# Performance work log

Hardware: AMD Instinct MI355X
Metric: run time of the kernel (lower is better)

## Reference

```python
import jax, jax.numpy as jnp
from jax import lax
import numpy as np

# Dims
B_, CIN, COUT, T = 2, 64, 128, 8192
K, NM, N, DCONV, EXP = 5, 2, 16, 4, 2   # kernel, n_mamba, d_state, d_conv, expand
DI = EXP * COUT                          # d_inner = 256
DTR = (COUT + 15) // 16                  # dt_rank = 8
M = NM * 2                               # mamba instances (fwd+bwd per block)


def setup_inputs() -> dict:
    key = jax.random.key(0)
    ks = jax.random.split(key, 8)
    r = lambda k, s, sc=0.02: (jax.random.normal(k, s) * sc).astype(jnp.float32)
    return {
        "x": jax.random.normal(ks[0], (B_, CIN, T), dtype=jnp.float32),
        "conv_w": r(ks[1], (COUT, CIN, K), 0.05),
        "conv_b": jnp.zeros((COUT,), jnp.float32),
        "gn_g": jnp.ones((COUT,), jnp.float32),
        "gn_b": jnp.zeros((COUT,), jnp.float32),
        "prelu_a": jnp.full((1,), 0.25, jnp.float32),
        "ln_g": jnp.ones((NM, COUT), jnp.float32),
        "ln_b": jnp.zeros((NM, COUT), jnp.float32),
        "W_in": r(ks[2], (M, 2 * DI, COUT)),
        "conv1d_w": r(ks[3], (M, DI, 1, DCONV), 0.1),
        "conv1d_b": jnp.zeros((M, DI), jnp.float32),
        "W_xproj": r(ks[4], (M, DTR + 2 * N, DI)),
        "W_dt": r(ks[5], (M, DI, DTR), 0.1),
        "b_dt": jnp.full((M, DI), -4.0, jnp.float32),
        "A_log": jnp.broadcast_to(jnp.log(jnp.arange(1, N + 1, dtype=jnp.float32)), (M, DI, N)).copy(),
        "D_param": jnp.ones((M, DI), jnp.float32),
        "W_out": r(ks[6], (M, COUT, DI)),
    }


def _silu(x):
    return x * jax.nn.sigmoid(x)


def _layernorm(x, g, b, eps=1e-5):
    mu = x.mean(-1, keepdims=True)
    v = ((x - mu) ** 2).mean(-1, keepdims=True)
    return (x - mu) * lax.rsqrt(v + eps) * g + b


def _mamba(h, Wi, cw, cb, Wx, Wd, bd, Alog, Dp, Wo):
    # h: [B, L, d_model] -> [B, L, d_model]. Standard Mamba (S6) block.
    Bb, L, _ = h.shape
    xz = jnp.einsum('bld,ed->ble', h, Wi)               # [B,L,2*DI]
    xp, z = jnp.split(xz, 2, axis=-1)
    xc = jnp.transpose(xp, (0, 2, 1))                   # [B,DI,L]
    xc = lax.conv_general_dilated(xc, cw, (1,), [(DCONV - 1, 0)],
                                  feature_group_count=DI,
                                  dimension_numbers=('NCH', 'OIH', 'NCH')) + cb[None, :, None]
    u = _silu(jnp.transpose(xc, (0, 2, 1)))             # [B,L,DI]
    xdbl = jnp.einsum('bld,ed->ble', u, Wx)             # [B,L,DTR+2N]
    dt, Bm, Cm = jnp.split(xdbl, [DTR, DTR + N], axis=-1)
    delta = jax.nn.softplus(jnp.einsum('blr,dr->bld', dt, Wd) + bd)  # [B,L,DI]
    A = -jnp.exp(Alog)                                  # [DI,N]
    dA = jnp.exp(delta[..., None] * A)                  # [B,L,DI,N]
    dBu = (delta * u)[..., None] * Bm[:, :, None, :]    # [B,L,DI,N]

    def step(hc, inp):
        a, b, c = inp
        hc = a * hc + b                                  # [B,DI,N]
        return hc, jnp.einsum('bdn,bn->bd', hc, c)

    h0 = jnp.zeros((Bb, DI, N), dtype=h.dtype)
    _, ys = lax.scan(step, h0, (jnp.moveaxis(dA, 1, 0), jnp.moveaxis(dBu, 1, 0), jnp.moveaxis(Cm, 1, 0)))
    y = jnp.moveaxis(ys, 0, 1) + u * Dp                 # [B,L,DI]
    y = y * _silu(z)
    return jnp.einsum('ble,de->bld', y, Wo)


def reference(x, conv_w, conv_b, gn_g, gn_b, prelu_a, ln_g, ln_b, W_in,
              conv1d_w, conv1d_b, W_xproj, W_dt, b_dt, A_log, D_param, W_out):
    # Conv1d stride 2, padding K//2: [B,CIN,T] -> [B,COUT,T//2]
    h = lax.conv_general_dilated(x, conv_w, (2,), [(K // 2, K // 2)],
                                 dimension_numbers=('NCH', 'OIH', 'NCH')) + conv_b[None, :, None]
    # GroupNorm(1, COUT): normalize jointly over (C, T)
    mu = h.mean((1, 2), keepdims=True)
    v = ((h - mu) ** 2).mean((1, 2), keepdims=True)
    h = (h - mu) * lax.rsqrt(v + 1e-5) * gn_g[None, :, None] + gn_b[None, :, None]
    h = jnp.where(h >= 0, h, prelu_a[0] * h)            # PReLU (shared scalar)
    h = jnp.transpose(h, (0, 2, 1))                     # [B, L, C]
    for i in range(NM):
        hn = _layernorm(h, ln_g[i], ln_b[i])
        f, bw = 2 * i, 2 * i + 1
        yf = _mamba(hn, W_in[f], conv1d_w[f], conv1d_b[f], W_xproj[f], W_dt[f], b_dt[f], A_log[f], D_param[f], W_out[f])
        hb = jnp.flip(hn, axis=1)
        yb = jnp.flip(_mamba(hb, W_in[bw], conv1d_w[bw], conv1d_b[bw], W_xproj[bw], W_dt[bw], b_dt[bw], A_log[bw], D_param[bw], W_out[bw]), axis=1)
        h = h + yf + yb                                  # bidirectional residual
    return jnp.transpose(h, (0, 2, 1))                   # [B, COUT, T//2]
```

## Files before the change

### kernel.cpp

```cpp
#include <hip/hip_runtime.h>
#include <hip/hip_bf16.h>
#include <math.h>

constexpr int B2   = 2;
constexpr int CIN  = 64;
constexpr int COUT = 128;
constexpr int T    = 8192;
constexpr int L    = 4096;
constexpr int DI   = 256;
constexpr int NST  = 16;
constexpr int DTR  = 8;
constexpr int Q    = 32;
constexpr int NC   = 128;
constexpr int TOK  = B2 * L;

typedef __attribute__((ext_vector_type(8))) short bf16x8s;
typedef __attribute__((ext_vector_type(4))) float f32x4;

__device__ __forceinline__ float sigmoidf_(float x) { return 1.f / (1.f + __expf(-x)); }
__device__ __forceinline__ unsigned short f2bf(float f) {
    unsigned int u = __float_as_uint(f);
    unsigned int r = (u + 0x7FFFu + ((u >> 16) & 1u)) >> 16;
    return (unsigned short)r;
}
__device__ __forceinline__ float bf2f(unsigned short s) {
    return __uint_as_float((unsigned int)s << 16);
}

__global__ __launch_bounds__(256) void prep_all_kernel(
    const float* __restrict__ W_in, const float* __restrict__ W_out,
    const float* __restrict__ cw,
    unsigned short* __restrict__ Winb, unsigned short* __restrict__ Woutb,
    unsigned short* __restrict__ Wrb, float* __restrict__ stats) {
    int idx = blockIdx.x * 256 + threadIdx.x;
    if (blockIdx.x == 0 && threadIdx.x < 4) stats[threadIdx.x] = 0.f;
    if (idx < 262144) {
        Winb[idx] = f2bf(W_in[idx]);
    } else if (idx < 393216) {
        int i = idx - 262144; Woutb[i] = f2bf(W_out[i]);
    } else if (idx < 434176) {
        int i = idx - 393216;
        int co = i / 320, r = i % 320;
        int kp = r >> 6, ci = r & 63;
        Wrb[i] = f2bf(cw[co * 320 + ci * 5 + kp]);
    }
}

__global__ __launch_bounds__(256) void xpose_kernel(
    const float* __restrict__ x, unsigned short* __restrict__ xTb) {
    __shared__ float tile[64][65];
    int b = blockIdx.y, tb = blockIdx.x * 64, tid = threadIdx.x;
    #pragma unroll
    for (int i = 0; i < 16; ++i) {
        int idx = i * 256 + tid; int ci = idx >> 6, tt = idx & 63;
        tile[ci][tt] = x[((size_t)b * CIN + ci) * T + tb + tt];
    }
    __syncthreads();
    #pragma unroll
    for (int i = 0; i < 16; ++i) {
        int idx = i * 256 + tid; int tt = idx >> 6, ci = idx & 63;
        xTb[((size_t)b * T + tb + tt) * 64 + ci] = f2bf(tile[ci][tt]);
    }
}

__global__ __launch_bounds__(256) void conv_mfma_kernel(
    const unsigned short* __restrict__ xTb, const unsigned short* __restrict__ Wrb,
    const float* __restrict__ cb, float* __restrict__ h, float* __restrict__ stats) {
    const int tid = threadIdx.x;
    const int w = tid >> 6, lane = tid & 63, q = lane >> 4, c = lane & 15;
    const int t0g = blockIdx.x * 64;
    const int t0  = t0g + w * 16;
    const int ct0 = blockIdx.y * 64;
    const int b   = t0g >> 12;
    const int l   = (t0 + c) & (L - 1);
    f32x4 acc[4] = {};
    for (int kc = 0; kc < 320; kc += 32) {
        int kp  = kc >> 6;
        int ci0 = (kc & 63) + q * 8;
        int p = 2 * l + kp - 2;
        bf16x8s a = {};
        if (p >= 0 && p < T)
            a = *(const bf16x8s*)&xTb[((size_t)b * T + p) * 64 + ci0];
        #pragma unroll
        for (int i = 0; i < 4; ++i) {
            bf16x8s bb = *(const bf16x8s*)&Wrb[(size_t)(ct0 + i * 16 + c) * 320 + kc + q * 8];
            acc[i] = __builtin_amdgcn_mfma_f32_16x16x32_bf16(a, bb, acc[i], 0, 0, 0);
        }
    }
    float s = 0.f, ss = 0.f;
    #pragma unroll
    for (int i = 0; i < 4; ++i) {
        int cout = ct0 + i * 16 + c;
        float bias = cb[cout];
        #pragma unroll
        for (int r = 0; r < 4; ++r) {
            int tok = t0 + q * 4 + r;
            float v = acc[i][r] + bias;
            h[(size_t)tok * COUT + cout] = v;
            s += v; ss += v * v;
        }
    }
    #pragma unroll
    for (int off = 32; off; off >>= 1) {
        s  += __shfl_down(s,  off, 64);
        ss += __shfl_down(ss, off, 64);
    }
    if (lane == 0) {
        atomicAdd(&stats[b * 2 + 0], s);
        atomicAdd(&stats[b * 2 + 1], ss);
    }
}

__global__ __launch_bounds__(256) void gn_ln_kernel(
    float* __restrict__ h, const float* __restrict__ gn_g,
    const float* __restrict__ gn_b, const float* __restrict__ prelu_a,
    const float* __restrict__ stats, unsigned short* __restrict__ hnb,
    const float* __restrict__ lng, const float* __restrict__ lnb) {
    int wave = threadIdx.x >> 6, lane = threadIdx.x & 63;
    int t = blockIdx.x * 4 + wave;
    int b = t >> 12;
    const float n = (float)(L * COUT);
    float mu   = stats[b * 2 + 0] / n;
    float var  = stats[b * 2 + 1] / n - mu * mu;
    float rstd = rsqrtf(var + 1e-5f);
    float a = prelu_a[0];
    float* row = h + (size_t)t * COUT;
    float2 v  = *(const float2*)&row[lane * 2];
    float2 g  = *(const float2*)&gn_g[lane * 2];
    float2 bb = *(const float2*)&gn_b[lane * 2];
    v.x = (v.x - mu) * rstd * g.x + bb.x; v.x = v.x >= 0.f ? v.x : a * v.x;
    v.y = (v.y - mu) * rstd * g.y + bb.y; v.y = v.y >= 0.f ? v.y : a * v.y;
    *(float2*)&row[lane * 2] = v;
    float s = v.x + v.y, ss = v.x * v.x + v.y * v.y;
    #pragma unroll
    for (int off = 32; off; off >>= 1) {
        s  += __shfl_xor(s,  off, 64);
        ss += __shfl_xor(ss, off, 64);
    }
    float mu2 = s * (1.f / 128.f);
    float var2 = ss * (1.f / 128.f) - mu2 * mu2;
    float rstd2 = rsqrtf(var2 + 1e-5f);
    float2 gg = *(const float2*)&lng[lane * 2];
    float2 lb = *(const float2*)&lnb[lane * 2];
    ushort2 o;
    o.x = f2bf((v.x - mu2) * rstd2 * gg.x + lb.x);
    o.y = f2bf((v.y - mu2) * rstd2 * gg.y + lb.y);
    *(ushort2*)&hnb[(size_t)t * COUT + lane * 2] = o;
}

__global__ __launch_bounds__(256) void ln_kernel(
    const float* __restrict__ h, unsigned short* __restrict__ hnb,
    const float* __restrict__ g, const float* __restrict__ bta) {
    int wave = threadIdx.x >> 6, lane = threadIdx.x & 63;
    int t = blockIdx.x * 4 + wave;
    const float* row = h + (size_t)t * COUT;
    float2 v = *(const float2*)&row[lane * 2];
    float s = v.x + v.y, ss = v.x * v.x + v.y * v.y;
    #pragma unroll
    for (int off = 32; off; off >>= 1) {
        s  += __shfl_xor(s,  off, 64);
        ss += __shfl_xor(ss, off, 64);
    }
    float mu = s * (1.f / 128.f);
    float var = ss * (1.f / 128.f) - mu * mu;
    float rstd = rsqrtf(var + 1e-5f);
    float2 gg = *(const float2*)&g[lane * 2];
    float2 bb = *(const float2*)&bta[lane * 2];
    ushort2 o;
    o.x = f2bf((v.x - mu) * rstd * gg.x + bb.x);
    o.y = f2bf((v.y - mu) * rstd * gg.y + bb.y);
    *(ushort2*)&hnb[(size_t)t * COUT + lane * 2] = o;
}

__global__ __launch_bounds__(256) void inproj_dw_kernel(
    const unsigned short* __restrict__ hnb, const unsigned short* __restrict__ Winb,
    const float* __restrict__ cw, const float* __restrict__ cbias,
    float* __restrict__ u0, float* __restrict__ u1,
    unsigned short* __restrict__ zb0, unsigned short* __restrict__ zb1, int layer) {
    __shared__ float xs[80 * 68];
    const int tid = threadIdx.x;
    const int w = tid >> 6, lane = tid & 63, q = lane >> 4, c = lane & 15;
    const int tBase = blockIdx.x * 64;
    const int nBase = blockIdx.y * 64;
    const int inst = nBase >> 9;
    const int e0 = nBase & 511;
    const int m = layer * 2 + inst;
    const unsigned short* Wb = Winb + (size_t)m * 512 * 128;

    if (e0 >= 256) {
        const int t0 = tBase + w * 16;
        f32x4 acc[4] = {};
        for (int kc = 0; kc < 128; kc += 32) {
            bf16x8s a = *(const bf16x8s*)&hnb[(size_t)(t0 + c) * 128 + kc + q * 8];
            #pragma unroll
            for (int i = 0; i < 4; ++i) {
                bf16x8s bb = *(const bf16x8s*)&Wb[(size_t)(e0 + i * 16 + c) * 128 + kc + q * 8];
                acc[i] = __builtin_amdgcn_mfma_f32_16x16x32_bf16(a, bb, acc[i], 0, 0, 0);
            }
        }
        unsigned short* zb = inst ? zb1 : zb0;
        #pragma unroll
        for (int i = 0; i < 4; ++i) {
            int eo = (e0 + i * 16 + c) & 255;
            #pragma unroll
            for (int r = 0; r < 4; ++r) {
                int tok = t0 + q * 4 + r;
                float v = acc[i][r];
                zb[(size_t)tok * DI + eo] = f2bf(v * sigmoidf_(v));
            }
        }
        return;
    }
    const int winT0 = (inst == 0) ? (tBase - 16) : tBase;
    for (int pass = 0; pass < 2; ++pass) {
        if (pass == 1 && w != 0) break;
        int slot = (pass == 0) ? (w + (inst == 0 ? 1 : 0))
                               : ((inst == 0) ? 0 : 4);
        int tokA = winT0 + slot * 16 + c;
        tokA = tokA < 0 ? 0 : (tokA > TOK - 1 ? TOK - 1 : tokA);
        f32x4 acc[4] = {};
        for (int kc = 0; kc < 128; kc += 32) {
            bf16x8s a = *(const bf16x8s*)&hnb[(size_t)tokA * 128 + kc + q * 8];
            #pragma unroll
            for (int i = 0; i < 4; ++i) {
                bf16x8s bb = *(const bf16x8s*)&Wb[(size_t)(e0 + i * 16 + c) * 128 + kc + q * 8];
                acc[i] = __builtin_amdgcn_mfma_f32_16x16x32_bf16(a, bb, acc[i], 0, 0, 0);
            }
        }
        #pragma unroll
        for (int i = 0; i < 4; ++i)
            #pragma unroll
            for (int r = 0; r < 4; ++r)
                xs[(slot * 16 + q * 4 + r) * 68 + i * 16 + c] = acc[i][r];
    }
    __syncthreads();
    const int l0base = tBase & (L - 1);
    const int ch4 = tid & 15;
    const int d0 = e0 + ch4 * 4;
    float4 w0 = *(const float4*)&cw[(size_t)(m * DI + d0 + 0) * 4];
    float4 w1 = *(const float4*)&cw[(size_t)(m * DI + d0 + 1) * 4];
    float4 w2 = *(const float4*)&cw[(size_t)(m * DI + d0 + 2) * 4];
    float4 w3 = *(const float4*)&cw[(size_t)(m * DI + d0 + 3) * 4];
    float4 bias4 = *(const float4*)&cbias[m * DI + d0];
    float* ud = inst ? u1 : u0;
    #pragma unroll
    for (int p = 0; p < 4; ++p) {
        int j = p * 16 + (tid >> 4);
        float4 acc = bias4;
        #pragma unroll
        for (int k = 0; k < 4; ++k) {
            bool valid = (inst == 0) ? (l0base + j - 3 + k >= 0)
                                     : (l0base + j + 3 - k < L);
            if (valid) {
                int wj = (inst == 0) ? (j + 13 + k) : (j + 3 - k);
                float4 v = *(const float4*)&xs[wj * 68 + ch4 * 4];
                float wk0 = ((const float*)&w0)[k], wk1 = ((const float*)&w1)[k];
                float wk2 = ((const float*)&w2)[k], wk3 = ((const float*)&w3)[k];
                acc.x = fmaf(wk0, v.x, acc.x); acc.y = fmaf(wk1, v.y, acc.y);
                acc.z = fmaf(wk2, v.z, acc.z); acc.w = fmaf(wk3, v.w, acc.w);
            }
        }
        acc.x *= sigmoidf_(acc.x); acc.y *= sigmoidf_(acc.y);
        acc.z *= sigmoidf_(acc.z); acc.w *= sigmoidf_(acc.w);
        *(float4*)&ud[(size_t)(tBase + j) * DI + d0] = acc;
    }
}

__global__ __launch_bounds__(256) void xproj_kernel(
    const float* __restrict__ u0, const float* __restrict__ u1,
    const float* __restrict__ Wx, const float* __restrict__ Wdt,
    const float* __restrict__ bdt,
    float* __restrict__ dl0, float* __restrict__ dl1,
    float* __restrict__ Bm0, float* __restrict__ Bm1,
    float* __restrict__ Cm0, float* __restrict__ Cm1, int layer) {
    __shared__ float Ws[40 * 132];
    __shared__ float As[128 * 33];
    __shared__ float xd[32 * 9];
    const int tid   = threadIdx.x;
    const int tBase = blockIdx.x * 32;
    const int inst  = blockIdx.y;
    const int m     = layer * 2 + inst;
    const float* u  = inst ? u1 : u0;
    const float* Wm = Wx + (size_t)m * 40 * 256;
    const int t  = tid & 31;
    const int eq = tid >> 5;
    float acc[5] = {};
    for (int kc = 0; kc < 256; kc += 128) {
        __syncthreads();
        #pragma unroll
        for (int i = 0; i < 5; ++i) {
            int idx = i * 256 + tid;
            int e = idx >> 5, kq = idx & 31;
            float4 w4 = *(const float4*)&Wm[(size_t)e * 256 + kc + kq * 4];
            float* dstw = &Ws[e * 132 + kq * 4];
            dstw[0] = w4.x; dstw[1] = w4.y; dstw[2] = w4.z; dstw[3] = w4.w;
        }
        #pragma unroll
        for (int i = 0; i < 4; ++i) {
            int flat = i * 256 + tid;
            int tt = flat >> 5, kq = flat & 31;
            float4 v = *(const float4*)&u[(size_t)(tBase + tt) * DI + kc + kq * 4];
            As[(kq * 4 + 0) * 33 + tt] = v.x;
            As[(kq * 4 + 1) * 33 + tt] = v.y;
            As[(kq * 4 + 2) * 33 + tt] = v.z;
            As[(kq * 4 + 3) * 33 + tt] = v.w;
        }
        __syncthreads();
        #pragma unroll 4
        for (int kk = 0; kk < 128; ++kk) {
            float a = As[kk * 33 + t];
            acc[0] = fmaf(a, Ws[(eq     ) * 132 + kk], acc[0]);
            acc[1] = fmaf(a, Ws[(eq +  8) * 132 + kk], acc[1]);
            acc[2] = fmaf(a, Ws[(eq + 16) * 132 + kk], acc[2]);
            acc[3] = fmaf(a, Ws[(eq + 24) * 132 + kk], acc[3]);
            acc[4] = fmaf(a, Ws[(eq + 32) * 132 + kk], acc[4]);
        }
    }
    {
        int tok = tBase + t;
        float* Bm = inst ? Bm1 : Bm0;
        float* Cm = inst ? Cm1 : Cm0;
        xd[t * 9 + eq] = acc[0];
        Bm[(size_t)tok * NST + eq]     = acc[1];
        Bm[(size_t)tok * NST + 8 + eq] = acc[2];
        Cm[(size_t)tok * NST + eq]     = acc[3];
        Cm[(size_t)tok * NST + 8 + eq] = acc[4];
    }
    __syncthreads();
    {
        int d = tid;
        float wr[8];
        #pragma unroll
        for (int r = 0; r < 8; ++r) wr[r] = Wdt[((size_t)m * DI + d) * DTR + r];
        float bb = bdt[m * DI + d];
        float* dl = inst ? dl1 : dl0;
        #pragma unroll 4
        for (int tt = 0; tt < 32; ++tt) {
            float a2 = bb;
            #pragma unroll
            for (int r = 0; r < 8; ++r) a2 = fmaf(xd[tt * 9 + r], wr[r], a2);
            float sp = fmaxf(a2, 0.f) + __logf(1.f + __expf(-fabsf(a2)));
            dl[(size_t)(tBase + tt) * DI + d] = sp;
        }
    }
}

__global__ __launch_bounds__(256) void scan1_kernel(
    const float* __restrict__ dl0, const float* __restrict__ dl1,
    const float* __restrict__ u0,  const float* __restrict__ u1,
    const float* __restrict__ Bm0, const float* __restrict__ Bm1,
    const float* __restrict__ A_log,
    float* __restrict__ hend, float* __restrict__ dsumb, int layer) {
    const int tid = threadIdx.x;
    const int nq = tid & 3, dlane = tid >> 2;
    const int chunk = blockIdx.x & (NC - 1), dtile = blockIdx.x >> 7;
    const int b = blockIdx.y, inst = blockIdx.z;
    const int m = layer * 2 + inst, dir = inst;
    const int d = dtile * 64 + dlane;
    const float* dl = inst ? dl1 : dl0;
    const float* u  = inst ? u1  : u0;
    const float* Bm = inst ? Bm1 : Bm0;
    float4 av = *(const float4*)&A_log[((size_t)m * DI + d) * NST + nq * 4];
    const float a0 = -expf(av.x), a1 = -expf(av.y), a2 = -expf(av.z), a3 = -expf(av.w);
    const int s0 = chunk * Q;
    const int l0 = dir ? (L - 1 - s0) : s0;
    const int stp = dir ? -1 : 1;
    long iDU = ((long)(b * L + l0)) * DI + d;
    int  iB  = ((b * L + l0) << 4) + nq * 4;
    const long sDU = (long)stp * DI;
    const int  sB  = stp * NST;
    float h0 = 0.f, h1 = 0.f, h2 = 0.f, h3 = 0.f, dsum = 0.f;
    #pragma unroll 4
    for (int t = 0; t < Q; ++t) {
        float dlt = dl[iDU], uu = u[iDU];
        float4 bm = *(const float4*)&Bm[iB];
        float du = dlt * uu;
        h0 = fmaf(__expf(dlt * a0), h0, du * bm.x);
        h1 = fmaf(__expf(dlt * a1), h1, du * bm.y);
        h2 = fmaf(__expf(dlt * a2), h2, du * bm.z);
        h3 = fmaf(__expf(dlt * a3), h3, du * bm.w);
        dsum += dlt;
        iDU += sDU; iB += sB;
    }
    size_t oh = (((size_t)(inst * 2 + b) * DI + d) * NC + chunk) * NST + nq * 4;
    *(float4*)&hend[oh] = make_float4(h0, h1, h2, h3);
    if (nq == 0) dsumb[((size_t)(inst * 2 + b) * NC + chunk) * DI + d] = dsum;
}

__global__ __launch_bounds__(256) void combine_kernel(
    float* __restrict__ hend, const float* __restrict__ dsumb,
    const float* __restrict__ A_log, int layer) {
    int flat = blockIdx.x * 256 + threadIdx.x;
    int n = flat & 15;
    int d = (flat >> 4) & 255;
    int b = (flat >> 12) & 1;
    int inst = flat >> 13;
    int m = layer * 2 + inst;
    float a = -expf(A_log[((size_t)m * DI + d) * NST + n]);
    size_t baseE = (((size_t)(inst * 2 + b) * DI + d) * NC) * NST + n;
    size_t baseD = ((size_t)(inst * 2 + b) * NC) * DI + d;
    float hc = 0.f;
    #pragma unroll 4
    for (int c = 0; c < NC; ++c) {
        float tmp = hend[baseE + (size_t)c * NST];
        hend[baseE + (size_t)c * NST] = hc;
        float ds = dsumb[baseD + (size_t)c * DI];
        hc = fmaf(__expf(a * ds), hc, tmp);
    }
}

__global__ __launch_bounds__(256) void scan2_kernel(
    const float* __restrict__ dl0, const float* __restrict__ dl1,
    const float* __restrict__ u0,  const float* __restrict__ u1,
    const float* __restrict__ Bm0, const float* __restrict__ Bm1,
    const float* __restrict__ Cm0, const float* __restrict__ Cm1,
    unsigned short* __restrict__ zb0, unsigned short* __restrict__ zb1,
    const float* __restrict__ hin, const float* __restrict__ A_log,
    const float* __restrict__ Dp, int layer) {
    const int tid = threadIdx.x;
    const int nq = tid & 3, dlane = tid >> 2;
    const int chunk = blockIdx.x & (NC - 1), dtile = blockIdx.x >> 7;
    const int b = blockIdx.y, inst = blockIdx.z;
    const int m = layer * 2 + inst, dir = inst;
    const int d = dtile * 64 + dlane;
    const float* dl = inst ? dl1 : dl0;
    const float* u  = inst ? u1  : u0;
    const float* Bm = inst ? Bm1 : Bm0;
    const float* Cm = inst ? Cm1 : Cm0;
    unsigned short* zs = inst ? zb1 : zb0;
    float4 av = *(const float4*)&A_log[((size_t)m * DI + d) * NST + nq * 4];
    const float a0 = -expf(av.x), a1 = -expf(av.y), a2 = -expf(av.z), a3 = -expf(av.w);
    const float dpar = Dp[m * DI + d];
    const int s0 = chunk * Q;
    const int l0 = dir ? (L - 1 - s0) : s0;
    const int stp = dir ? -1 : 1;
    long iDU = ((long)(b * L + l0)) * DI + d;
    int  iB  = ((b * L + l0) << 4) + nq * 4;
    const long sDU = (long)stp * DI;
    const int  sB  = stp * NST;
    float4 hv = *(const float4*)&hin[(((size_t)(inst * 2 + b) * DI + d) * NC + chunk) * NST + nq * 4];
    float h0 = hv.x, h1 = hv.y, h2 = hv.z, h3 = hv.w;
    #pragma unroll 4
    for (int t = 0; t < Q; ++t) {
        float dlt = dl[iDU], uu = u[iDU];
        float4 bm = *(const float4*)&Bm[iB];
        float4 cm = *(const float4*)&Cm[iB];
        float du = dlt * uu;
        h0 = fmaf(__expf(dlt * a0), h0, du * bm.x);
        h1 = fmaf(__expf(dlt * a1), h1, du * bm.y);
        h2 = fmaf(__expf(dlt * a2), h2, du * bm.z);
        h3 = fmaf(__expf(dlt * a3), h3, du * bm.w);
        float yp = h0 * cm.x + h1 * cm.y + h2 * cm.z + h3 * cm.w;
        yp += __shfl_xor(yp, 1, 4);
        yp += __shfl_xor(yp, 2, 4);
        if (nq == 0) {
            float zv = bf2f(zs[iDU]);
            zs[iDU] = f2bf(fmaf(uu, dpar, yp) * zv);
        }
        iDU += sDU; iB += sB;
    }
}

__global__ __launch_bounds__(256) void outproj_mfma_kernel(
    const unsigned short* __restrict__ ygb0, const unsigned short* __restrict__ ygb1,
    const unsigned short* __restrict__ Woutb, float* __restrict__ h, int layer) {
    const int tid = threadIdx.x;
    const int w = tid >> 6, lane = tid & 63, q = lane >> 4, c = lane & 15;
    const int t0 = blockIdx.x * 64 + w * 16;
    const int ct0 = blockIdx.y * 32;
    f32x4 acc[2] = {};
    #pragma unroll
    for (int inst = 0; inst < 2; ++inst) {
        const unsigned short* yg = inst ? ygb1 : ygb0;
        const unsigned short* Wb = Woutb + (size_t)(layer * 2 + inst) * COUT * DI;
        for (int kc = 0; kc < 256; kc += 32) {
            bf16x8s a = *(const bf16x8s*)&yg[(size_t)(t0 + c) * DI + kc + q * 8];
            #pragma unroll
            for (int i = 0; i < 2; ++i) {
                bf16x8s bb = *(const bf16x8s*)&Wb[(size_t)(ct0 + i * 16 + c) * DI + kc + q * 8];
                acc[i] = __builtin_amdgcn_mfma_f32_16x16x32_bf16(a, bb, acc[i], 0, 0, 0);
            }
        }
    }
    #pragma unroll
    for (int i = 0; i < 2; ++i) {
        int cout = ct0 + i * 16 + c;
        #pragma unroll
        for (int r = 0; r < 4; ++r) {
            int tok = t0 + q * 4 + r;
            h[(size_t)tok * COUT + cout] += acc[i][r];
        }
    }
}

__global__ __launch_bounds__(256) void transpose_kernel(
    const float* __restrict__ h, float* __restrict__ out) {
    __shared__ float tile[32][33];
    int lt0 = blockIdx.x * 32, ct0 = blockIdx.y * 32, b = blockIdx.z;
    int c = threadIdx.x & 31, r = threadIdx.x >> 5;
    #pragma unroll
    for (int j = 0; j < 4; ++j) {
        int ll = r + 8 * j;
        tile[ll][c] = h[((size_t)b * L + lt0 + ll) * COUT + ct0 + c];
    }
    __syncthreads();
    #pragma unroll
    for (int j = 0; j < 4; ++j) {
        int cc = r + 8 * j;
        out[((size_t)b * COUT + ct0 + cc) * L + lt0 + c] = tile[c][cc];
    }
}

extern "C" void kernel_launch(void* const* d_in, const int* in_sizes, int n_in,
                              void* d_out, int out_size, void* d_ws, size_t ws_size,
                              hipStream_t stream) {
    const float* x        = (const float*)d_in[0];
    const float* conv_w   = (const float*)d_in[1];
    const float* conv_b   = (const float*)d_in[2];
    const float* gn_g     = (const float*)d_in[3];
    const float* gn_b     = (const float*)d_in[4];
    const float* prelu_a  = (const float*)d_in[5];
    const float* ln_g     = (const float*)d_in[6];
    const float* ln_b     = (const float*)d_in[7];
    const float* W_in     = (const float*)d_in[8];
    const float* conv1d_w = (const float*)d_in[9];
    const float* conv1d_b = (const float*)d_in[10];
    const float* W_xproj  = (const float*)d_in[11];
    const float* W_dt     = (const float*)d_in[12];
    const float* b_dt     = (const float*)d_in[13];
    const float* A_log    = (const float*)d_in[14];
    const float* D_param  = (const float*)d_in[15];
    const float* W_out    = (const float*)d_in[16];

    float* ws = (float*)d_ws;
    float* h     = ws;
    unsigned short* zb0 = (unsigned short*)(ws + 5242880);
    unsigned short* zb1 = (unsigned short*)(ws + 6291456);
    float* u0    = ws + 7340032;
    float* u1    = ws + 9437184;
    float* dl0   = ws + 11534336;
    float* dl1   = ws + 13631488;
    float* Bm0   = ws + 15728640;
    float* Bm1   = ws + 15859712;
    float* Cm0   = ws + 15990784;
    float* Cm1   = ws + 16121856;
    float* hend  = ws + 16252928;
    float* dsumb = ws + 18350080;
    unsigned short* Winb  = (unsigned short*)(ws + 18481152);
    unsigned short* Wrb   = (unsigned short*)(ws + 18612224);
    unsigned short* Woutb = (unsigned short*)(ws + 18632704);
    float* stats = ws + 18698240;
    unsigned short* hnb = (unsigned short*)hend;
    unsigned short* xTb = zb0;

    prep_all_kernel<<<1696, 256, 0, stream>>>(W_in, W_out, conv_w, Winb, Woutb, Wrb, stats);
    xpose_kernel<<<dim3(T / 64, B2), 256, 0, stream>>>(x, xTb);
    conv_mfma_kernel<<<dim3(TOK / 64, COUT / 64), 256, 0, stream>>>(xTb, Wrb, conv_b, h, stats);
    gn_ln_kernel<<<TOK / 4, 256, 0, stream>>>(h, gn_g, gn_b, prelu_a, stats, hnb, ln_g, ln_b);

    for (int layer = 0; layer < 2; ++layer) {
        if (layer == 1)
            ln_kernel<<<TOK / 4, 256, 0, stream>>>(h, hnb, ln_g + COUT, ln_b + COUT);
        inproj_dw_kernel<<<dim3(TOK / 64, 16), 256, 0, stream>>>(hnb, Winb, conv1d_w, conv1d_b,
                                                                 u0, u1, zb0, zb1, layer);
        xproj_kernel<<<dim3(TOK / 32, 2), 256, 0, stream>>>(u0, u1, W_xproj, W_dt, b_dt,
                                                            dl0, dl1, Bm0, Bm1, Cm0, Cm1, layer);
        scan1_kernel<<<dim3(NC * 4, B2, 2), 256, 0, stream>>>(dl0, dl1, u0, u1, Bm0, Bm1,
                                                              A_log, hend, dsumb, layer);
        combine_kernel<<<64, 256, 0, stream>>>(hend, dsumb, A_log, layer);
        scan2_kernel<<<dim3(NC * 4, B2, 2), 256, 0, stream>>>(dl0, dl1, u0, u1, Bm0, Bm1, Cm0, Cm1,
                                                              zb0, zb1, hend, A_log, D_param, layer);
        outproj_mfma_kernel<<<dim3(TOK / 64, 4), 256, 0, stream>>>(zb0, zb1, Woutb, h, layer);
    }
    transpose_kernel<<<dim3(L / 32, COUT / 32, B2), 256, 0, stream>>>(h, (float*)d_out);
}
```

Baseline: 379.8 us.

## Recompute delta in scan kernels, restructure xproj, fuse final transpose into outproj

The xproj kernel no longer materialises the full [TOK, DI] softplus delta tensor. It writes only the 8-wide dt-rank projection, and both scan kernels recompute delta per chunk in shared memory from xd, W_dt and b_dt. This removes a large write and two large reads of delta per layer, at the cost of duplicated softplus work in scan1 and scan2. The xproj GEMM is also rewritten to read operands directly from global memory with register tiling and a split-K reduction in shared memory. The last layer's outproj writes the transposed output directly, which drops the separate transpose kernel.

```diff
diff --git a/kernel.cpp b/kernel.cpp
--- a/kernel.cpp
+++ b/kernel.cpp
@@ -268,103 +268,128 @@
 
 __global__ __launch_bounds__(256) void xproj_kernel(
     const float* __restrict__ u0, const float* __restrict__ u1,
-    const float* __restrict__ Wx, const float* __restrict__ Wdt,
-    const float* __restrict__ bdt,
-    float* __restrict__ dl0, float* __restrict__ dl1,
+    const float* __restrict__ Wx,
+    float* __restrict__ xd0, float* __restrict__ xd1,
     float* __restrict__ Bm0, float* __restrict__ Bm1,
     float* __restrict__ Cm0, float* __restrict__ Cm1, int layer) {
-    __shared__ float Ws[40 * 132];
-    __shared__ float As[128 * 33];
-    __shared__ float xd[32 * 9];
+    __shared__ float red[4][64][21];
     const int tid   = threadIdx.x;
+    const int kq    = tid >> 6;
+    const int lane  = tid & 63;
+    const int eq    = lane & 7;
+    const int tq    = lane >> 3;
     const int tBase = blockIdx.x * 32;
     const int inst  = blockIdx.y;
     const int m     = layer * 2 + inst;
     const float* u  = inst ? u1 : u0;
     const float* Wm = Wx + (size_t)m * 40 * 256;
-    const int t  = tid & 31;
-    const int eq = tid >> 5;
-    float acc[5] = {};
-    for (int kc = 0; kc < 256; kc += 128) {
-        __syncthreads();
-        #pragma unroll
-        for (int i = 0; i < 5; ++i) {
-            int idx = i * 256 + tid;
-            int e = idx >> 5, kq = idx & 31;
-            float4 w4 = *(const float4*)&Wm[(size_t)e * 256 + kc + kq * 4];
-            float* dstw = &Ws[e * 132 + kq * 4];
-            dstw[0] = w4.x; dstw[1] = w4.y; dstw[2] = w4.z; dstw[3] = w4.w;
-        }
-        #pragma unroll
-        for (int i = 0; i < 4; ++i) {
-            int flat = i * 256 + tid;
-            int tt = flat >> 5, kq = flat & 31;
-            float4 v = *(const float4*)&u[(size_t)(tBase + tt) * DI + kc + kq * 4];
-            As[(kq * 4 + 0) * 33 + tt] = v.x;
-            As[(kq * 4 + 1) * 33 + tt] = v.y;
-            As[(kq * 4 + 2) * 33 + tt] = v.z;
-            As[(kq * 4 + 3) * 33 + tt] = v.w;
-        }
-        __syncthreads();
-        #pragma unroll 4
-        for (int kk = 0; kk < 128; ++kk) {
-            float a = As[kk * 33 + t];
-            acc[0] = fmaf(a, Ws[(eq     ) * 132 + kk], acc[0]);
-            acc[1] = fmaf(a, Ws[(eq +  8) * 132 + kk], acc[1]);
-            acc[2] = fmaf(a, Ws[(eq + 16) * 132 + kk], acc[2]);
-            acc[3] = fmaf(a, Ws[(eq + 24) * 132 + kk], acc[3]);
-            acc[4] = fmaf(a, Ws[(eq + 32) * 132 + kk], acc[4]);
-        }
-    }
+    const int k0 = kq * 64;
+    const float* uB = u + (size_t)(tBase + tq * 4) * 256 + k0;
+    float acc[5][4] = {};
+    #pragma unroll 2
+    for (int kk = 0; kk < 64; kk += 4) {
+        float4 a[4], w[5];
+        #pragma unroll
+        for (int j = 0; j < 4; ++j)
+            a[j] = *(const float4*)&uB[(size_t)j * 256 + kk];
+        #pragma unroll
+        for (int i = 0; i < 5; ++i)
+            w[i] = *(const float4*)&Wm[(size_t)(eq + i * 8) * 256 + k0 + kk];
+        #pragma unroll
+        for (int i = 0; i < 5; ++i)
+            #pragma unroll
+            for (int j = 0; j < 4; ++j) {
+                acc[i][j] = fmaf(a[j].x, w[i].x, acc[i][j]);
+                acc[i][j] = fmaf(a[j].y, w[i].y, acc[i][j]);
+                acc[i][j] = fmaf(a[j].z, w[i].z, acc[i][j]);
+                acc[i][j] = fmaf(a[j].w, w[i].w, acc[i][j]);
+            }
+    }
+    #pragma unroll
+    for (int i = 0; i < 5; ++i)
+        #pragma unroll
+        for (int j = 0; j < 4; ++j)
+            red[kq][lane][i * 4 + j] = acc[i][j];
+    __syncthreads();
+    if (kq != 0) return;
+    #pragma unroll
+    for (int i = 0; i < 5; ++i)
+        #pragma unroll
+        for (int j = 0; j < 4; ++j)
+            acc[i][j] = red[0][lane][i * 4 + j] + red[1][lane][i * 4 + j]
+                      + red[2][lane][i * 4 + j] + red[3][lane][i * 4 + j];
+    float* xd = inst ? xd1 : xd0;
+    float* Bm = inst ? Bm1 : Bm0;
+    float* Cm = inst ? Cm1 : Cm0;
+    #pragma unroll
+    for (int j = 0; j < 4; ++j) {
+        int tok = tBase + tq * 4 + j;
+        xd[(size_t)tok * DTR + eq]       = acc[0][j];
+        Bm[(size_t)tok * NST + eq]       = acc[1][j];
+        Bm[(size_t)tok * NST + 8 + eq]   = acc[2][j];
+        Cm[(size_t)tok * NST + eq]       = acc[3][j];
+        Cm[(size_t)tok * NST + 8 + eq]   = acc[4][j];
+    }
+}
+
+__device__ __forceinline__ void compute_dls(
+    const float* __restrict__ xd, const float* __restrict__ Wdt,
+    const float* __restrict__ bdt, int m, int dtile, int b, int l0, int stp,
+    float* dls, float* xdL, float* WdtL, float* bdtL) {
+    const int tid = threadIdx.x;
     {
-        int tok = tBase + t;
-        float* Bm = inst ? Bm1 : Bm0;
-        float* Cm = inst ? Cm1 : Cm0;
-        xd[t * 9 + eq] = acc[0];
-        Bm[(size_t)tok * NST + eq]     = acc[1];
-        Bm[(size_t)tok * NST + 8 + eq] = acc[2];
-        Cm[(size_t)tok * NST + eq]     = acc[3];
-        Cm[(size_t)tok * NST + 8 + eq] = acc[4];
+        int j = tid >> 3, r = tid & 7;
+        xdL[j * 9 + r] = xd[(size_t)(b * L + l0 + stp * j) * DTR + r];
+        size_t wbase = ((size_t)m * DI + dtile * 64) * DTR;
+        WdtL[tid]       = Wdt[wbase + tid];
+        WdtL[tid + 256] = Wdt[wbase + tid + 256];
+        if (tid < 64) bdtL[tid] = bdt[m * DI + dtile * 64 + tid];
     }
     __syncthreads();
     {
-        int d = tid;
-        float wr[8];
-        #pragma unroll
-        for (int r = 0; r < 8; ++r) wr[r] = Wdt[((size_t)m * DI + d) * DTR + r];
-        float bb = bdt[m * DI + d];
-        float* dl = inst ? dl1 : dl0;
-        #pragma unroll 4
-        for (int tt = 0; tt < 32; ++tt) {
-            float a2 = bb;
-            #pragma unroll
-            for (int r = 0; r < 8; ++r) a2 = fmaf(xd[tt * 9 + r], wr[r], a2);
+        int tt = tid & 31, dgrp = tid >> 5;
+        float xr[8];
+        #pragma unroll
+        for (int r = 0; r < 8; ++r) xr[r] = xdL[tt * 9 + r];
+        #pragma unroll
+        for (int i = 0; i < 8; ++i) {
+            int dd = dgrp * 8 + i;
+            float a2 = bdtL[dd];
+            #pragma unroll
+            for (int r = 0; r < 8; ++r) a2 = fmaf(xr[r], WdtL[dd * 8 + r], a2);
             float sp = fmaxf(a2, 0.f) + __logf(1.f + __expf(-fabsf(a2)));
-            dl[(size_t)(tBase + tt) * DI + d] = sp;
-        }
-    }
+            dls[tt * 69 + dd] = sp;
+        }
+    }
+    __syncthreads();
 }
 
 __global__ __launch_bounds__(256) void scan1_kernel(
-    const float* __restrict__ dl0, const float* __restrict__ dl1,
+    const float* __restrict__ xd0, const float* __restrict__ xd1,
     const float* __restrict__ u0,  const float* __restrict__ u1,
     const float* __restrict__ Bm0, const float* __restrict__ Bm1,
+    const float* __restrict__ Wdt, const float* __restrict__ bdt,
     const float* __restrict__ A_log,
     float* __restrict__ hend, float* __restrict__ dsumb, int layer) {
+    __shared__ float dls[32 * 69];
+    __shared__ float xdL[32 * 9];
+    __shared__ float WdtL[512];
+    __shared__ float bdtL[64];
     const int tid = threadIdx.x;
     const int nq = tid & 3, dlane = tid >> 2;
     const int chunk = blockIdx.x & (NC - 1), dtile = blockIdx.x >> 7;
     const int b = blockIdx.y, inst = blockIdx.z;
     const int m = layer * 2 + inst, dir = inst;
     const int d = dtile * 64 + dlane;
-    const float* dl = inst ? dl1 : dl0;
+    const float* xd = inst ? xd1 : xd0;
     const float* u  = inst ? u1  : u0;
     const float* Bm = inst ? Bm1 : Bm0;
-    float4 av = *(const float4*)&A_log[((size_t)m * DI + d) * NST + nq * 4];
-    const float a0 = -expf(av.x), a1 = -expf(av.y), a2 = -expf(av.z), a3 = -expf(av.w);
     const int s0 = chunk * Q;
     const int l0 = dir ? (L - 1 - s0) : s0;
     const int stp = dir ? -1 : 1;
+    compute_dls(xd, Wdt, bdt, m, dtile, b, l0, stp, dls, xdL, WdtL, bdtL);
+    float4 av = *(const float4*)&A_log[((size_t)m * DI + d) * NST + nq * 4];
+    const float a0 = -expf(av.x), a1 = -expf(av.y), a2 = -expf(av.z), a3 = -expf(av.w);
     long iDU = ((long)(b * L + l0)) * DI + d;
     int  iB  = ((b * L + l0) << 4) + nq * 4;
     const long sDU = (long)stp * DI;
@@ -372,7 +397,7 @@
     float h0 = 0.f, h1 = 0.f, h2 = 0.f, h3 = 0.f, dsum = 0.f;
     #pragma unroll 4
     for (int t = 0; t < Q; ++t) {
-        float dlt = dl[iDU], uu = u[iDU];
+        float dlt = dls[t * 69 + dlane], uu = u[iDU];
         float4 bm = *(const float4*)&Bm[iB];
         float du = dlt * uu;
         h0 = fmaf(__expf(dlt * a0), h0, du * bm.x);
@@ -410,30 +435,36 @@
 }
 
 __global__ __launch_bounds__(256) void scan2_kernel(
-    const float* __restrict__ dl0, const float* __restrict__ dl1,
+    const float* __restrict__ xd0, const float* __restrict__ xd1,
     const float* __restrict__ u0,  const float* __restrict__ u1,
     const float* __restrict__ Bm0, const float* __restrict__ Bm1,
     const float* __restrict__ Cm0, const float* __restrict__ Cm1,
     unsigned short* __restrict__ zb0, unsigned short* __restrict__ zb1,
-    const float* __restrict__ hin, const float* __restrict__ A_log,
+    const float* __restrict__ hin, const float* __restrict__ Wdt,
+    const float* __restrict__ bdt, const float* __restrict__ A_log,
     const float* __restrict__ Dp, int layer) {
+    __shared__ float dls[32 * 69];
+    __shared__ float xdL[32 * 9];
+    __shared__ float WdtL[512];
+    __shared__ float bdtL[64];
     const int tid = threadIdx.x;
     const int nq = tid & 3, dlane = tid >> 2;
     const int chunk = blockIdx.x & (NC - 1), dtile = blockIdx.x >> 7;
     const int b = blockIdx.y, inst = blockIdx.z;
     const int m = layer * 2 + inst, dir = inst;
     const int d = dtile * 64 + dlane;
-    const float* dl = inst ? dl1 : dl0;
+    const float* xd = inst ? xd1 : xd0;
     const float* u  = inst ? u1  : u0;
     const float* Bm = inst ? Bm1 : Bm0;
     const float* Cm = inst ? Cm1 : Cm0;
     unsigned short* zs = inst ? zb1 : zb0;
+    const int s0 = chunk * Q;
+    const int l0 = dir ? (L - 1 - s0) : s0;
+    const int stp = dir ? -1 : 1;
+    compute_dls(xd, Wdt, bdt, m, dtile, b, l0, stp, dls, xdL, WdtL, bdtL);
     float4 av = *(const float4*)&A_log[((size_t)m * DI + d) * NST + nq * 4];
     const float a0 = -expf(av.x), a1 = -expf(av.y), a2 = -expf(av.z), a3 = -expf(av.w);
     const float dpar = Dp[m * DI + d];
-    const int s0 = chunk * Q;
-    const int l0 = dir ? (L - 1 - s0) : s0;
-    const int stp = dir ? -1 : 1;
     long iDU = ((long)(b * L + l0)) * DI + d;
     int  iB  = ((b * L + l0) << 4) + nq * 4;
     const long sDU = (long)stp * DI;
@@ -442,7 +473,7 @@
     float h0 = hv.x, h1 = hv.y, h2 = hv.z, h3 = hv.w;
     #pragma unroll 4
     for (int t = 0; t < Q; ++t) {
-        float dlt = dl[iDU], uu = u[iDU];
+        float dlt = dls[t * 69 + dlane], uu = u[iDU];
         float4 bm = *(const float4*)&Bm[iB];
         float4 cm = *(const float4*)&Cm[iB];
         float du = dlt * uu;
@@ -463,7 +494,8 @@
 
 __global__ __launch_bounds__(256) void outproj_mfma_kernel(
     const unsigned short* __restrict__ ygb0, const unsigned short* __restrict__ ygb1,
-    const unsigned short* __restrict__ Woutb, float* __restrict__ h, int layer) {
+    const unsigned short* __restrict__ Woutb, float* __restrict__ h,
+    float* __restrict__ out, int layer) {
     const int tid = threadIdx.x;
     const int w = tid >> 6, lane = tid & 63, q = lane >> 4, c = lane & 15;
     const int t0 = blockIdx.x * 64 + w * 16;
@@ -482,32 +514,29 @@
             }
         }
     }
-    #pragma unroll
-    for (int i = 0; i < 2; ++i) {
-        int cout = ct0 + i * 16 + c;
-        #pragma unroll
-        for (int r = 0; r < 4; ++r) {
-            int tok = t0 + q * 4 + r;
-            h[(size_t)tok * COUT + cout] += acc[i][r];
-        }
-    }
-}
-
-__global__ __launch_bounds__(256) void transpose_kernel(
-    const float* __restrict__ h, float* __restrict__ out) {
-    __shared__ float tile[32][33];
-    int lt0 = blockIdx.x * 32, ct0 = blockIdx.y * 32, b = blockIdx.z;
-    int c = threadIdx.x & 31, r = threadIdx.x >> 5;
-    #pragma unroll
-    for (int j = 0; j < 4; ++j) {
-        int ll = r + 8 * j;
-        tile[ll][c] = h[((size_t)b * L + lt0 + ll) * COUT + ct0 + c];
-    }
-    __syncthreads();
-    #pragma unroll
-    for (int j = 0; j < 4; ++j) {
-        int cc = r + 8 * j;
-        out[((size_t)b * COUT + ct0 + cc) * L + lt0 + c] = tile[c][cc];
+    if (layer == 0) {
+        #pragma unroll
+        for (int i = 0; i < 2; ++i) {
+            int cout = ct0 + i * 16 + c;
+            #pragma unroll
+            for (int r = 0; r < 4; ++r) {
+                int tok = t0 + q * 4 + r;
+                h[(size_t)tok * COUT + cout] += acc[i][r];
+            }
+        }
+    } else {
+        int tok0 = t0 + q * 4;
+        int b = tok0 >> 12, l = tok0 & (L - 1);
+        #pragma unroll
+        for (int i = 0; i < 2; ++i) {
+            int cout = ct0 + i * 16 + c;
+            float4 o;
+            o.x = h[(size_t)(tok0 + 0) * COUT + cout] + acc[i][0];
+            o.y = h[(size_t)(tok0 + 1) * COUT + cout] + acc[i][1];
+            o.z = h[(size_t)(tok0 + 2) * COUT + cout] + acc[i][2];
+            o.w = h[(size_t)(tok0 + 3) * COUT + cout] + acc[i][3];
+            *(float4*)&out[((size_t)(b * COUT + cout)) * L + l] = o;
+        }
     }
 }
 
@@ -538,8 +567,8 @@
     unsigned short* zb1 = (unsigned short*)(ws + 6291456);
     float* u0    = ws + 7340032;
     float* u1    = ws + 9437184;
-    float* dl0   = ws + 11534336;
-    float* dl1   = ws + 13631488;
+    float* xd0   = ws + 11534336;
+    float* xd1   = ws + 11599872;
     float* Bm0   = ws + 15728640;
     float* Bm1   = ws + 15859712;
     float* Cm0   = ws + 15990784;
@@ -552,6 +581,7 @@
     float* stats = ws + 18698240;
     unsigned short* hnb = (unsigned short*)hend;
     unsigned short* xTb = zb0;
+    float* out = (float*)d_out;
 
     prep_all_kernel<<<1696, 256, 0, stream>>>(W_in, W_out, conv_w, Winb, Woutb, Wrb, stats);
     xpose_kernel<<<dim3(T / 64, B2), 256, 0, stream>>>(x, xTb);
@@ -563,14 +593,14 @@
             ln_kernel<<<TOK / 4, 256, 0, stream>>>(h, hnb, ln_g + COUT, ln_b + COUT);
         inproj_dw_kernel<<<dim3(TOK / 64, 16), 256, 0, stream>>>(hnb, Winb, conv1d_w, conv1d_b,
                                                                  u0, u1, zb0, zb1, layer);
-        xproj_kernel<<<dim3(TOK / 32, 2), 256, 0, stream>>>(u0, u1, W_xproj, W_dt, b_dt,
-                                                            dl0, dl1, Bm0, Bm1, Cm0, Cm1, layer);
-        scan1_kernel<<<dim3(NC * 4, B2, 2), 256, 0, stream>>>(dl0, dl1, u0, u1, Bm0, Bm1,
-                                                              A_log, hend, dsumb, layer);
+        xproj_kernel<<<dim3(TOK / 32, 2), 256, 0, stream>>>(u0, u1, W_xproj,
+                                                            xd0, xd1, Bm0, Bm1, Cm0, Cm1, layer);
+        scan1_kernel<<<dim3(NC * 4, B2, 2), 256, 0, stream>>>(xd0, xd1, u0, u1, Bm0, Bm1,
+                                                              W_dt, b_dt, A_log, hend, dsumb, layer);
         combine_kernel<<<64, 256, 0, stream>>>(hend, dsumb, A_log, layer);
-        scan2_kernel<<<dim3(NC * 4, B2, 2), 256, 0, stream>>>(dl0, dl1, u0, u1, Bm0, Bm1, Cm0, Cm1,
-                                                              zb0, zb1, hend, A_log, D_param, layer);
-        outproj_mfma_kernel<<<dim3(TOK / 64, 4), 256, 0, stream>>>(zb0, zb1, Woutb, h, layer);
-    }
-    transpose_kernel<<<dim3(L / 32, COUT / 32, B2), 256, 0, stream>>>(h, (float*)d_out);
-}
+        scan2_kernel<<<dim3(NC * 4, B2, 2), 256, 0, stream>>>(xd0, xd1, u0, u1, Bm0, Bm1, Cm0, Cm1,
+                                                              zb0, zb1, hend, W_dt, b_dt,
+                                                              A_log, D_param, layer);
+        outproj_mfma_kernel<<<dim3(TOK / 64, 4), 256, 0, stream>>>(zb0, zb1, Woutb, h, out, layer);
+    }
+}
```

New measurement: 395.9 us. 1.04x slower.
